# Kernel tuning notes

Hardware: AMD Instinct MI355X
Metric: run time of the kernel (lower is better)

The kernel has to match this reference:

```python
import jax, jax.numpy as jnp
import numpy as np

DIM = 1024
NUM_HEADS = 16
DIM_HEAD = 64
INNER = NUM_HEADS * DIM_HEAD  # 1024
SCALE = DIM_HEAD ** -0.5


def setup_inputs() -> dict:
    key = jax.random.key(0)
    ks = jax.random.split(key, 8)
    B, SQ, SK = 2, 2048, 4096
    x = jax.random.normal(ks[0], (B, SQ, DIM), dtype=jnp.float32)
    context = jax.random.normal(ks[1], (B, SK, DIM), dtype=jnp.float32)
    # LayerNorm params
    ln_gamma = jnp.ones((DIM,), jnp.float32)
    ln_beta = jnp.zeros((DIM,), jnp.float32)
    # Linear weights, stored as [in, out] so y = x @ W (torch Linear weight transposed)
    w_q = jax.random.normal(ks[2], (DIM, INNER), dtype=jnp.float32) / np.sqrt(DIM)
    w_kv = jax.random.normal(ks[3], (DIM, 2 * INNER), dtype=jnp.float32) / np.sqrt(DIM)
    w_out = jax.random.normal(ks[4], (INNER, DIM), dtype=jnp.float32) / np.sqrt(INNER)
    b_out = jnp.zeros((DIM,), jnp.float32)
    # torch init is 0.0 (tanh(0)=0); use a nonzero value so output/grads are nontrivial
    gate = jnp.array([0.5], jnp.float32)
    return {"x": x, "context": context, "ln_gamma": ln_gamma, "ln_beta": ln_beta,
            "w_q": w_q, "w_kv": w_kv, "w_out": w_out, "b_out": b_out, "gate": gate}


def _layernorm(x, gamma, beta, eps=1e-5):
    mu = jnp.mean(x, axis=-1, keepdims=True)
    var = jnp.mean(jnp.square(x - mu), axis=-1, keepdims=True)
    return (x - mu) * jax.lax.rsqrt(var + eps) * gamma + beta


def reference(x, context, ln_gamma, ln_beta, w_q, w_kv, w_out, b_out, gate):
    B, SQ, _ = x.shape
    SK = context.shape[1]
    xn = _layernorm(x, ln_gamma, ln_beta)
    q = (xn @ w_q).reshape(B, SQ, NUM_HEADS, DIM_HEAD)
    kv = context @ w_kv
    k, v = jnp.split(kv, 2, axis=-1)
    k = k.reshape(B, SK, NUM_HEADS, DIM_HEAD)
    v = v.reshape(B, SK, NUM_HEADS, DIM_HEAD)
    # scores: [B, H, SQ, SK]
    scores = jnp.einsum('bqhd,bkhd->bhqk', q * SCALE, k)
    attn = jax.nn.softmax(scores, axis=-1)
    out = jnp.einsum('bhqk,bkhd->bqhd', attn, v).reshape(B, SQ, INNER)
    out = out @ w_out + b_out
    return out * jnp.tanh(gate[0])
```

## Files before the change

### kernel.cpp

```cpp
#include <hip/hip_runtime.h>
#include <hip/hip_bf16.h>
#include <stdint.h>

#define DIMM  1024
#define NHEAD 16
#define DHEAD 64
#define BB    2
#define SQL   2048
#define SKL   4096
#define KVW   2048
#define NT    (SKL / 64)

typedef __attribute__((ext_vector_type(8))) short short8;
typedef __attribute__((ext_vector_type(4))) float f32x4;
typedef __attribute__((ext_vector_type(16))) float f32x16;
typedef __attribute__((ext_vector_type(4))) unsigned short us4;

typedef const __attribute__((address_space(1))) uint32_t gu32_t;
typedef __attribute__((address_space(3))) uint32_t lu32_t;

#define GLDS16(gp, lp) __builtin_amdgcn_global_load_lds((gu32_t*)(gp), (lu32_t*)(lp), 16, 0, 0)

static __device__ __forceinline__ unsigned short f2bf(float f) {
  union { float f; uint32_t u; } v; v.f = f;
  uint32_t r = v.u + 0x7fffu + ((v.u >> 16) & 1u);
  return (unsigned short)(r >> 16);
}

__global__ __launch_bounds__(256) void k_wprep(const float* __restrict__ wq,
                                               const float* __restrict__ wkv,
                                               const float* __restrict__ wot,
                                               unsigned short* __restrict__ WQT,
                                               unsigned short* __restrict__ WKVT,
                                               unsigned short* __restrict__ WOT) {
  __shared__ float tile[32][33];
  const int bid = blockIdx.x;
  const float* in; unsigned short* out; int N, bx, by;
  if (bid < 1024)      {               in = wq;  out = WQT;  N = 1024; bx = bid & 31; by = bid >> 5; }
  else if (bid < 3072) { int l = bid - 1024; in = wkv; out = WKVT; N = 2048; bx = l & 63; by = l >> 6; }
  else                 { int l = bid - 3072; in = wot; out = WOT;  N = 1024; bx = l & 31; by = l >> 5; }
  const int K = 1024;
  const int n0 = bx * 32, k0 = by * 32;
  const int tx = threadIdx.x, ty = threadIdx.y;
  #pragma unroll
  for (int i = 0; i < 4; i++)
    tile[ty + i * 8][tx] = in[(size_t)(k0 + ty + i * 8) * N + n0 + tx];
  __syncthreads();
  #pragma unroll
  for (int i = 0; i < 4; i++)
    out[(size_t)(n0 + ty + i * 8) * K + k0 + tx] = f2bf(tile[tx][ty + i * 8]);
}

__global__ __launch_bounds__(256) void k_ln(const float* __restrict__ x,
                                            const float* __restrict__ gamma,
                                            const float* __restrict__ beta,
                                            unsigned short* __restrict__ out) {
  const int row = blockIdx.x, tid = threadIdx.x;
  const float* xr = x + (size_t)row * DIMM;
  float4 v = *(const float4*)(xr + tid * 4);
  float s = v.x + v.y + v.z + v.w;
  float ss = v.x * v.x + v.y * v.y + v.z * v.z + v.w * v.w;
  #pragma unroll
  for (int m = 1; m < 64; m <<= 1) {
    s += __shfl_xor(s, m);
    ss += __shfl_xor(ss, m);
  }
  __shared__ float red[8];
  const int wid = tid >> 6, lane = tid & 63;
  if (lane == 0) { red[wid] = s; red[4 + wid] = ss; }
  __syncthreads();
  s = red[0] + red[1] + red[2] + red[3];
  ss = red[4] + red[5] + red[6] + red[7];
  float mu = s * (1.0f / DIMM);
  float var = ss * (1.0f / DIMM) - mu * mu;
  float rstd = rsqrtf(var + 1e-5f);
  float4 g = *(const float4*)(gamma + tid * 4);
  float4 bt = *(const float4*)(beta + tid * 4);
  us4 o;
  o.x = f2bf((v.x - mu) * rstd * g.x + bt.x);
  o.y = f2bf((v.y - mu) * rstd * g.y + bt.y);
  o.z = f2bf((v.z - mu) * rstd * g.z + bt.z);
  o.w = f2bf((v.w - mu) * rstd * g.w + bt.w);
  *(us4*)(out + (size_t)row * DIMM + tid * 4) = o;
}

__global__ __launch_bounds__(256) void k_proj(const float* __restrict__ ctx,
                                              const unsigned short* __restrict__ XN,
                                              const unsigned short* __restrict__ WKVT,
                                              const unsigned short* __restrict__ WQT,
                                              unsigned short* __restrict__ KVB,
                                              unsigned short* __restrict__ QB) {
  __shared__ unsigned short lA[2][128 * 32];
  __shared__ unsigned short lB[2][128 * 32];
  const int tid = threadIdx.x;
  const int wid = tid >> 6, lane = tid & 63;
  const int kg = lane >> 4, lr = lane & 15;
  const int wr = wid >> 1, wc = wid & 1;
  const int K = 1024, nt = 32;

  const int bid = blockIdx.x;
  const int xcd = bid & 7;
  const int idx = bid >> 3;
  const bool isQ = (idx >= 128);
  int im, in_, N;
  const unsigned short* Bw;
  unsigned short* Cout;
  if (isQ) { int q = idx - 128; im = xcd * 4 + (q & 3); in_ = q >> 2; Bw = WQT;  Cout = QB;  N = 1024; }
  else     {                    im = xcd * 8 + (idx & 7); in_ = idx >> 3; Bw = WKVT; Cout = KVB; N = 2048; }
  const size_t baseB = (size_t)in_ * 128 * K;
  const unsigned short* Abf = XN + (size_t)im * 128 * K;
  const float* Af = ctx + (size_t)im * 128 * K;

  int ed[2], grow[2], gcol[2];
  #pragma unroll
  for (int j = 0; j < 2; j++) {
    int e = wid * 1024 + j * 512 + lane * 8;
    ed[j] = e;
    int row = e >> 5;
    grow[j] = row;
    gcol[j] = (((e >> 3) & 3) ^ ((row >> 1) & 3)) << 3;
  }
  uint32_t awoff[4];
  #pragma unroll
  for (int p = 0; p < 4; p++) {
    int row = p * 32 + (tid >> 3);
    int g = (tid & 7) >> 1;
    awoff[p] = (uint32_t)(row * 64 + ((g ^ ((row >> 1) & 3)) << 4) + (tid & 1) * 8);
  }

  f32x4 acc[4][4];
  #pragma unroll
  for (int m = 0; m < 4; m++)
    #pragma unroll
    for (int n = 0; n < 4; n++) {
      f32x4 z = {0.0f, 0.0f, 0.0f, 0.0f};
      acc[m][n] = z;
    }

  float4 va[4];
  auto STAGE_B = [&](int bufi, int t) {
    int k0 = t << 5;
    #pragma unroll
    for (int j = 0; j < 2; j++)
      GLDS16(Bw + baseB + (size_t)grow[j] * K + k0 + gcol[j], &lB[bufi][ed[j]]);
  };
  auto STAGE_A_Q = [&](int bufi, int t) {
    int k0 = t << 5;
    #pragma unroll
    for (int j = 0; j < 2; j++)
      GLDS16(Abf + (size_t)grow[j] * K + k0 + gcol[j], &lA[bufi][ed[j]]);
  };
  auto LOAD_A_F32 = [&](int t) {
    int k0 = t << 5;
    #pragma unroll
    for (int p = 0; p < 4; p++)
      va[p] = *(const float4*)(Af + (size_t)(p * 32 + (tid >> 3)) * K + k0 + (tid & 7) * 4);
  };
  auto WRITE_A_F32 = [&](int bufi) {
    #pragma unroll
    for (int p = 0; p < 4; p++) {
      uint32_t lo, hi;
      asm("v_cvt_pk_bf16_f32 %0, %1, %2" : "=v"(lo) : "v"(va[p].x), "v"(va[p].y));
      asm("v_cvt_pk_bf16_f32 %0, %1, %2" : "=v"(hi) : "v"(va[p].z), "v"(va[p].w));
      uint2 w2; w2.x = lo; w2.y = hi;
      *(uint2*)((char*)&lA[bufi][0] + awoff[p]) = w2;
    }
  };
  auto COMPUTE = [&](int bufi) {
    short8 a[4], b[4];
    #pragma unroll
    for (int m = 0; m < 4; m++) {
      int row = wr * 64 + m * 16 + lr;
      a[m] = *(const short8*)&lA[bufi][row * 32 + ((kg ^ ((row >> 1) & 3)) << 3)];
    }
    #pragma unroll
    for (int n = 0; n < 4; n++) {
      int row = wc * 64 + n * 16 + lr;
      b[n] = *(const short8*)&lB[bufi][row * 32 + ((kg ^ ((row >> 1) & 3)) << 3)];
    }
    #pragma unroll
    for (int m = 0; m < 4; m++)
      #pragma unroll
      for (int n = 0; n < 4; n++)
        acc[m][n] = __builtin_amdgcn_mfma_f32_16x16x32_bf16(a[m], b[n], acc[m][n], 0, 0, 0);
  };

  int buf = 0;
  if (isQ) {
    STAGE_A_Q(0, 0); STAGE_B(0, 0);
    __syncthreads();
    for (int t = 0; t < nt; t++) {
      if (t + 1 < nt) { STAGE_A_Q(buf ^ 1, t + 1); STAGE_B(buf ^ 1, t + 1); }
      COMPUTE(buf);
      __syncthreads();
      buf ^= 1;
    }
  } else {
    LOAD_A_F32(0); STAGE_B(0, 0); WRITE_A_F32(0);
    __syncthreads();
    for (int t = 0; t < nt; t++) {
      if (t + 1 < nt) { LOAD_A_F32(t + 1); STAGE_B(buf ^ 1, t + 1); }
      COMPUTE(buf);
      if (t + 1 < nt) WRITE_A_F32(buf ^ 1);
      __syncthreads();
      buf ^= 1;
    }
  }

  const int r0 = im * 128 + wr * 64;
  const int c0 = in_ * 128 + wc * 64;
  #pragma unroll
  for (int m = 0; m < 4; m++)
    #pragma unroll
    for (int n = 0; n < 4; n++)
      #pragma unroll
      for (int j = 0; j < 4; j++)
        Cout[(size_t)(r0 + m * 16 + kg * 4 + j) * N + c0 + n * 16 + lr] = f2bf(acc[m][n][j]);
}

__global__ __launch_bounds__(256) void k_out(const unsigned short* __restrict__ A,
                                             const unsigned short* __restrict__ BT,
                                             float* __restrict__ C,
                                             const float* __restrict__ bias,
                                             const float* __restrict__ gate) {
  __shared__ unsigned short lA[2][64 * 32];
  __shared__ unsigned short lB[2][128 * 32];
  const int tid = threadIdx.x;
  const int wid = tid >> 6, lane = tid & 63;
  const int kg = lane >> 4, lr = lane & 15;
  const int wr = wid >> 1, wc = wid & 1;
  const int K = 1024, nt = 32, N = 1024;

  const int bid = blockIdx.x;
  const int xcd = bid & 7;
  const int idx = bid >> 3;
  const int im = xcd * 8 + (idx & 7);
  const int in_ = idx >> 3;
  const size_t baseA = (size_t)im * 64 * K;
  const size_t baseB = (size_t)in_ * 128 * K;

  int eA, arow, acol;
  {
    int e = tid * 8;
    eA = e;
    int row = e >> 5;
    arow = row; acol = (((e >> 3) & 3) ^ ((row >> 1) & 3)) << 3;
  }
  int eB[2], brow[2], bcol[2];
  #pragma unroll
  for (int j = 0; j < 2; j++) {
    int e = tid * 8 + j * 2048;
    eB[j] = e;
    int row = e >> 5;
    brow[j] = row; bcol[j] = (((e >> 3) & 3) ^ ((row >> 1) & 3)) << 3;
  }

  f32x4 acc[2][4];
  #pragma unroll
  for (int m = 0; m < 2; m++)
    #pragma unroll
    for (int n = 0; n < 4; n++) {
      f32x4 z = {0.0f, 0.0f, 0.0f, 0.0f};
      acc[m][n] = z;
    }

  auto STAGE = [&](int bufi, int t) {
    int k0 = t << 5;
    GLDS16(A + baseA + (size_t)arow * K + k0 + acol, &lA[bufi][eA]);
    #pragma unroll
    for (int j = 0; j < 2; j++)
      GLDS16(BT + baseB + (size_t)brow[j] * K + k0 + bcol[j], &lB[bufi][eB[j]]);
  };

  STAGE(0, 0);
  __syncthreads();
  int buf = 0;
  for (int t = 0; t < nt; t++) {
    if (t + 1 < nt) STAGE(buf ^ 1, t + 1);
    short8 a[2], b[4];
    #pragma unroll
    for (int m = 0; m < 2; m++) {
      int row = wr * 32 + m * 16 + lr;
      a[m] = *(const short8*)&lA[buf][row * 32 + ((kg ^ ((row >> 1) & 3)) << 3)];
    }
    #pragma unroll
    for (int n = 0; n < 4; n++) {
      int row = wc * 64 + n * 16 + lr;
      b[n] = *(const short8*)&lB[buf][row * 32 + ((kg ^ ((row >> 1) & 3)) << 3)];
    }
    #pragma unroll
    for (int m = 0; m < 2; m++)
      #pragma unroll
      for (int n = 0; n < 4; n++)
        acc[m][n] = __builtin_amdgcn_mfma_f32_16x16x32_bf16(a[m], b[n], acc[m][n], 0, 0, 0);
    __syncthreads();
    buf ^= 1;
  }

  const int r0 = im * 64 + wr * 32;
  const int c0 = in_ * 128 + wc * 64;
  float gl = tanhf(gate[0]);
  #pragma unroll
  for (int m = 0; m < 2; m++)
    #pragma unroll
    for (int n = 0; n < 4; n++)
      #pragma unroll
      for (int j = 0; j < 4; j++) {
        int col = c0 + n * 16 + lr;
        C[(size_t)(r0 + m * 16 + kg * 4 + j) * N + col] = (acc[m][n][j] + bias[col]) * gl;
      }
}

__global__ __launch_bounds__(256, 4) void k_attn(const unsigned short* __restrict__ Q,
                                                 const unsigned short* __restrict__ KV,
                                                 unsigned short* __restrict__ O) {
  __shared__ unsigned short sK[2][64 * 64];
  __shared__ unsigned short sV[2][64 * 64];

  const int tid = threadIdx.x;
  const int wave = tid >> 6, lane = tid & 63;
  const int wq = wave & 1, wk = wave >> 1;
  const int l31 = lane & 31, hi = lane >> 5;

  const int wid_b = blockIdx.x;
  const int work = (wid_b & 7) * 128 + (wid_b >> 3);
  const int qb = work & 31, bh = work >> 5;
  const int b = bh >> 4, h = bh & 15;

  const unsigned short* Qp = Q + (size_t)b * SQL * DIMM + h * DHEAD;
  const unsigned short* Kp = KV + (size_t)b * SKL * KVW + h * DHEAD;
  const unsigned short* Vp = Kp + DIMM;

  const int qr0 = qb * 64 + wq * 32;

  const unsigned short* ksrc[2]; int kdst[2];
  const unsigned short* vsrc[2]; int vdst[2];
  #pragma unroll
  for (int j = 0; j < 2; j++) {
    int e = (tid + j * 256) * 8;
    int row = e >> 6;
    int col = (((e >> 3) & 7) ^ (row & 7)) << 3;
    ksrc[j] = Kp + (size_t)row * KVW + col;
    kdst[j] = e;
    int g = tid + j * 256;
    int key = (g >> 5) * 4 + ((g >> 1) & 3);
    int d0v = ((g >> 3) & 3) * 16 + (g & 1) * 8;
    vsrc[j] = Vp + (size_t)key * KVW + d0v;
    vdst[j] = g * 8;
  }

  auto STAGE = [&](int bufi, int kt) {
    size_t off = (size_t)kt * 64 * KVW;
    #pragma unroll
    for (int j = 0; j < 2; j++) GLDS16(ksrc[j] + off, &sK[bufi][kdst[j]]);
    #pragma unroll
    for (int j = 0; j < 2; j++) GLDS16(vsrc[j] + off, &sV[bufi][vdst[j]]);
  };

  short8 qa[4];
  #pragma unroll
  for (int t = 0; t < 4; t++) {
    short8 v = *(const short8*)(Qp + (size_t)(qr0 + l31) * DIMM + t * 16 + hi * 8);
    #pragma unroll
    for (int j = 0; j < 8; j++) {
      union { float f; uint32_t u; } c;
      c.u = ((uint32_t)(unsigned short)v[j]) << 16;
      v[j] = (short)f2bf(c.f * 0.1803368801111f);
    }
    qa[t] = v;
  }

  f32x16 oacc[2];
  #pragma unroll
  for (int d2 = 0; d2 < 2; d2++)
    #pragma unroll
    for (int r = 0; r < 16; r++) oacc[d2][r] = 0.0f;
  float rs = 0.0f;

  const uint32_t sVb0 = (uint32_t)(size_t)(lu32_t*)&sV[0][0] +
                        (uint32_t)(hi * 1024 + ((lane >> 4) & 1) * 128 + (lane & 15) * 8);

  STAGE(0, 0);
  __syncthreads();

  union u4s8 { uint32_t u[4]; short8 s; };

  int buf = 0;
  for (int kt = 0; kt < NT; kt++) {
    if (kt + 1 < NT) STAGE(buf ^ 1, kt + 1);

    short8 kbf[4];
    {
      int row = wk * 32 + l31;
      #pragma unroll
      for (int t = 0; t < 4; t++) {
        int gl = t * 2 + hi;
        kbf[t] = *(const short8*)&sK[buf][row * 64 + ((gl ^ (row & 7)) << 3)];
      }
    }

    f32x16 sc;
    #pragma unroll
    for (int r = 0; r < 16; r++) sc[r] = 0.0f;
    #pragma unroll
    for (int t = 0; t < 4; t++)
      sc = __builtin_amdgcn_mfma_f32_32x32x16_bf16(kbf[t], qa[t], sc, 0, 0, 0);

    float p[16];
    #pragma unroll
    for (int r = 0; r < 16; r++) {
      p[r] = __builtin_amdgcn_exp2f(sc[r]);
      rs += p[r];
    }
    uint32_t w[8];
    #pragma unroll
    for (int i = 0; i < 8; i++)
      asm("v_cvt_pk_bf16_f32 %0, %1, %2" : "=v"(w[i]) : "v"(p[2 * i]), "v"(p[2 * i + 1]));
    asm("v_permlane32_swap_b32 %0, %1" : "+v"(w[0]), "+v"(w[2]));
    asm("v_permlane32_swap_b32 %0, %1" : "+v"(w[1]), "+v"(w[3]));
    asm("v_permlane32_swap_b32 %0, %1" : "+v"(w[4]), "+v"(w[6]));
    asm("v_permlane32_swap_b32 %0, %1" : "+v"(w[5]), "+v"(w[7]));
    u4s8 paf[2];
    paf[0].u[0] = w[0]; paf[0].u[1] = w[1]; paf[0].u[2] = w[2]; paf[0].u[3] = w[3];
    paf[1].u[0] = w[4]; paf[1].u[1] = w[5]; paf[1].u[2] = w[6]; paf[1].u[3] = w[7];

    u4s8 vb[2][2];
    {
      uint32_t tb = sVb0 + (uint32_t)(buf * 8192 + wk * 4096);
      #pragma unroll
      for (int d2 = 0; d2 < 2; d2++)
        #pragma unroll
        for (int ks = 0; ks < 2; ks++) {
          uint2 t0, t1;
          uint32_t a0 = tb + (uint32_t)(ks * 2048 + d2 * 256);
          asm volatile("ds_read_b64_tr_b16 %0, %1" : "=v"(t0) : "v"(a0));
          asm volatile("ds_read_b64_tr_b16 %0, %1" : "=v"(t1) : "v"(a0 + 512u));
          vb[d2][ks].u[0] = t0.x; vb[d2][ks].u[1] = t0.y;
          vb[d2][ks].u[2] = t1.x; vb[d2][ks].u[3] = t1.y;
        }
    }
    asm volatile("s_waitcnt lgkmcnt(0)" ::: "memory");
    __builtin_amdgcn_sched_barrier(0);

    #pragma unroll
    for (int d2 = 0; d2 < 2; d2++)
      #pragma unroll
      for (int ks = 0; ks < 2; ks++)
        oacc[d2] = __builtin_amdgcn_mfma_f32_32x32x16_bf16(paf[ks].s, vb[d2][ks].s, oacc[d2], 0, 0, 0);

    __syncthreads();
    buf ^= 1;
  }

  float* sRed = (float*)&sK[0][0];
  float* sRs  = (float*)&sV[0][0];
  if (wk == 1) {
    #pragma unroll
    for (int d2 = 0; d2 < 2; d2++)
      #pragma unroll
      for (int r = 0; r < 16; r++)
        sRed[((wq * 2 + d2) * 16 + r) * 64 + lane] = oacc[d2][r];
    sRs[wq * 64 + lane] = rs;
  }
  __syncthreads();
  if (wk == 0) {
    #pragma unroll
    for (int d2 = 0; d2 < 2; d2++)
      #pragma unroll
      for (int r = 0; r < 16; r++)
        oacc[d2][r] += sRed[((wq * 2 + d2) * 16 + r) * 64 + lane];
    float rs2 = rs + sRs[wq * 64 + lane];
    float t = rs2 + __shfl_xor(rs2, 32);
    float inv = 1.0f / t;
    float rq[16];
    #pragma unroll
    for (int r = 0; r < 16; r++) {
      int rho = (r & 3) + 8 * (r >> 2) + 4 * hi;
      rq[r] = __shfl(inv, rho);
    }
    unsigned short* Op = O + (size_t)b * SQL * DIMM + h * DHEAD;
    #pragma unroll
    for (int d2 = 0; d2 < 2; d2++)
      #pragma unroll
      for (int r = 0; r < 16; r++) {
        int rho = (r & 3) + 8 * (r >> 2) + 4 * hi;
        Op[(size_t)(qr0 + rho) * DIMM + d2 * 32 + l31] = f2bf(oacc[d2][r] * rq[r]);
      }
  }
}

extern "C" void kernel_launch(void* const* d_in, const int* in_sizes, int n_in,
                              void* d_out, int out_size, void* d_ws, size_t ws_size,
                              hipStream_t stream) {
  (void)in_sizes; (void)n_in; (void)out_size; (void)ws_size;
  const float* x     = (const float*)d_in[0];
  const float* ctx   = (const float*)d_in[1];
  const float* gamma = (const float*)d_in[2];
  const float* beta  = (const float*)d_in[3];
  const float* w_q   = (const float*)d_in[4];
  const float* w_kv  = (const float*)d_in[5];
  const float* w_out = (const float*)d_in[6];
  const float* b_out = (const float*)d_in[7];
  const float* gate  = (const float*)d_in[8];
  float* out = (float*)d_out;
  char* ws = (char*)d_ws;

  unsigned short* XN   = (unsigned short*)(ws);
  unsigned short* QB   = (unsigned short*)(ws + (8ull  << 20));
  unsigned short* KVB  = (unsigned short*)(ws + (32ull << 20));
  unsigned short* OB   = (unsigned short*)(ws + (64ull << 20));
  unsigned short* WQT  = (unsigned short*)(ws + (72ull << 20));
  unsigned short* WKVT = (unsigned short*)(ws + (74ull << 20));
  unsigned short* WOT  = (unsigned short*)(ws + (78ull << 20));

  k_wprep<<<dim3(4096), dim3(32, 8), 0, stream>>>(w_q, w_kv, w_out, WQT, WKVT, WOT);
  k_ln<<<dim3(4096), dim3(256), 0, stream>>>(x, gamma, beta, XN);
  k_proj<<<dim3(1280), dim3(256), 0, stream>>>(ctx, XN, WKVT, WQT, KVB, QB);
  k_attn<<<dim3(1024), dim3(256), 0, stream>>>(QB, KVB, OB);
  k_out<<<dim3(512), dim3(256), 0, stream>>>(OB, WOT, out, b_out, gate);
}
```

Before: 206.0 us.

## Merge prep kernels and pre-convert context to bf16 for uniform projection path

Combines weight transpose, layernorm, and a new context fp32-to-bf16 conversion into one prep launch, removing a kernel launch. The KV projection then stages its A operand with direct global-to-LDS bf16 loads instead of register fp32 loads plus in-loop conversion, so both projection paths share one pipeline. The cost is an extra write and read of a 16 MB bf16 context buffer through global memory.

```diff
diff --git a/kernel.cpp b/kernel.cpp
--- a/kernel.cpp
+++ b/kernel.cpp
@@ -27,64 +27,77 @@
   return (unsigned short)(r >> 16);
 }
 
-__global__ __launch_bounds__(256) void k_wprep(const float* __restrict__ wq,
-                                               const float* __restrict__ wkv,
-                                               const float* __restrict__ wot,
-                                               unsigned short* __restrict__ WQT,
-                                               unsigned short* __restrict__ WKVT,
-                                               unsigned short* __restrict__ WOT) {
-  __shared__ float tile[32][33];
+__global__ __launch_bounds__(256) void k_prep(const float* __restrict__ wq,
+                                              const float* __restrict__ wkv,
+                                              const float* __restrict__ wot,
+                                              const float* __restrict__ x,
+                                              const float* __restrict__ gamma,
+                                              const float* __restrict__ beta,
+                                              const float* __restrict__ ctx,
+                                              unsigned short* __restrict__ WQT,
+                                              unsigned short* __restrict__ WKVT,
+                                              unsigned short* __restrict__ WOT,
+                                              unsigned short* __restrict__ XN,
+                                              unsigned short* __restrict__ CTXB) {
   const int bid = blockIdx.x;
-  const float* in; unsigned short* out; int N, bx, by;
-  if (bid < 1024)      {               in = wq;  out = WQT;  N = 1024; bx = bid & 31; by = bid >> 5; }
-  else if (bid < 3072) { int l = bid - 1024; in = wkv; out = WKVT; N = 2048; bx = l & 63; by = l >> 6; }
-  else                 { int l = bid - 3072; in = wot; out = WOT;  N = 1024; bx = l & 31; by = l >> 5; }
-  const int K = 1024;
-  const int n0 = bx * 32, k0 = by * 32;
-  const int tx = threadIdx.x, ty = threadIdx.y;
-  #pragma unroll
-  for (int i = 0; i < 4; i++)
-    tile[ty + i * 8][tx] = in[(size_t)(k0 + ty + i * 8) * N + n0 + tx];
-  __syncthreads();
-  #pragma unroll
-  for (int i = 0; i < 4; i++)
-    out[(size_t)(n0 + ty + i * 8) * K + k0 + tx] = f2bf(tile[tx][ty + i * 8]);
-}
-
-__global__ __launch_bounds__(256) void k_ln(const float* __restrict__ x,
-                                            const float* __restrict__ gamma,
-                                            const float* __restrict__ beta,
-                                            unsigned short* __restrict__ out) {
-  const int row = blockIdx.x, tid = threadIdx.x;
-  const float* xr = x + (size_t)row * DIMM;
-  float4 v = *(const float4*)(xr + tid * 4);
-  float s = v.x + v.y + v.z + v.w;
-  float ss = v.x * v.x + v.y * v.y + v.z * v.z + v.w * v.w;
-  #pragma unroll
-  for (int m = 1; m < 64; m <<= 1) {
-    s += __shfl_xor(s, m);
-    ss += __shfl_xor(ss, m);
-  }
-  __shared__ float red[8];
-  const int wid = tid >> 6, lane = tid & 63;
-  if (lane == 0) { red[wid] = s; red[4 + wid] = ss; }
-  __syncthreads();
-  s = red[0] + red[1] + red[2] + red[3];
-  ss = red[4] + red[5] + red[6] + red[7];
-  float mu = s * (1.0f / DIMM);
-  float var = ss * (1.0f / DIMM) - mu * mu;
-  float rstd = rsqrtf(var + 1e-5f);
-  float4 g = *(const float4*)(gamma + tid * 4);
-  float4 bt = *(const float4*)(beta + tid * 4);
-  us4 o;
-  o.x = f2bf((v.x - mu) * rstd * g.x + bt.x);
-  o.y = f2bf((v.y - mu) * rstd * g.y + bt.y);
-  o.z = f2bf((v.z - mu) * rstd * g.z + bt.z);
-  o.w = f2bf((v.w - mu) * rstd * g.w + bt.w);
-  *(us4*)(out + (size_t)row * DIMM + tid * 4) = o;
-}
-
-__global__ __launch_bounds__(256) void k_proj(const float* __restrict__ ctx,
+  const int tid = threadIdx.x;
+
+  if (bid < 4096) {
+    __shared__ float tile[32][33];
+    const float* in; unsigned short* out; int N, bx, by;
+    if (bid < 1024)      {                    in = wq;  out = WQT;  N = 1024; bx = bid & 31; by = bid >> 5; }
+    else if (bid < 3072) { int l = bid - 1024; in = wkv; out = WKVT; N = 2048; bx = l & 63; by = l >> 6; }
+    else                 { int l = bid - 3072; in = wot; out = WOT;  N = 1024; bx = l & 31; by = l >> 5; }
+    const int K = 1024;
+    const int n0 = bx * 32, k0 = by * 32;
+    const int tx = tid & 31, ty = tid >> 5;
+    #pragma unroll
+    for (int i = 0; i < 4; i++)
+      tile[ty + i * 8][tx] = in[(size_t)(k0 + ty + i * 8) * N + n0 + tx];
+    __syncthreads();
+    #pragma unroll
+    for (int i = 0; i < 4; i++)
+      out[(size_t)(n0 + ty + i * 8) * K + k0 + tx] = f2bf(tile[tx][ty + i * 8]);
+  } else if (bid < 8192) {
+    const int row = bid - 4096;
+    const float* xr = x + (size_t)row * DIMM;
+    float4 v = *(const float4*)(xr + tid * 4);
+    float s = v.x + v.y + v.z + v.w;
+    float ss = v.x * v.x + v.y * v.y + v.z * v.z + v.w * v.w;
+    #pragma unroll
+    for (int m = 1; m < 64; m <<= 1) {
+      s += __shfl_xor(s, m);
+      ss += __shfl_xor(ss, m);
+    }
+    __shared__ float red[8];
+    const int wid = tid >> 6, lane = tid & 63;
+    if (lane == 0) { red[wid] = s; red[4 + wid] = ss; }
+    __syncthreads();
+    s = red[0] + red[1] + red[2] + red[3];
+    ss = red[4] + red[5] + red[6] + red[7];
+    float mu = s * (1.0f / DIMM);
+    float var = ss * (1.0f / DIMM) - mu * mu;
+    float rstd = rsqrtf(var + 1e-5f);
+    float4 g = *(const float4*)(gamma + tid * 4);
+    float4 bt = *(const float4*)(beta + tid * 4);
+    us4 o;
+    o.x = f2bf((v.x - mu) * rstd * g.x + bt.x);
+    o.y = f2bf((v.y - mu) * rstd * g.y + bt.y);
+    o.z = f2bf((v.z - mu) * rstd * g.z + bt.z);
+    o.w = f2bf((v.w - mu) * rstd * g.w + bt.w);
+    *(us4*)(XN + (size_t)row * DIMM + tid * 4) = o;
+  } else {
+    size_t i = ((size_t)(bid - 8192) * 256 + tid) * 8;
+    float4 v0 = *(const float4*)(ctx + i);
+    float4 v1 = *(const float4*)(ctx + i + 4);
+    union { us4 h[2]; short8 s; } o;
+    o.h[0].x = f2bf(v0.x); o.h[0].y = f2bf(v0.y); o.h[0].z = f2bf(v0.z); o.h[0].w = f2bf(v0.w);
+    o.h[1].x = f2bf(v1.x); o.h[1].y = f2bf(v1.y); o.h[1].z = f2bf(v1.z); o.h[1].w = f2bf(v1.w);
+    *(short8*)(CTXB + i) = o.s;
+  }
+}
+
+__global__ __launch_bounds__(256) void k_proj(const unsigned short* __restrict__ CTXB,
                                               const unsigned short* __restrict__ XN,
                                               const unsigned short* __restrict__ WKVT,
                                               const unsigned short* __restrict__ WQT,
@@ -103,13 +116,13 @@
   const int idx = bid >> 3;
   const bool isQ = (idx >= 128);
   int im, in_, N;
+  const unsigned short* Ap;
   const unsigned short* Bw;
   unsigned short* Cout;
-  if (isQ) { int q = idx - 128; im = xcd * 4 + (q & 3); in_ = q >> 2; Bw = WQT;  Cout = QB;  N = 1024; }
-  else     {                    im = xcd * 8 + (idx & 7); in_ = idx >> 3; Bw = WKVT; Cout = KVB; N = 2048; }
+  if (isQ) { int q = idx - 128; im = xcd * 4 + (q & 3);   in_ = q >> 2;   Bw = WQT;  Cout = QB;  N = 1024; Ap = XN; }
+  else     {                    im = xcd * 8 + (idx & 7); in_ = idx >> 3; Bw = WKVT; Cout = KVB; N = 2048; Ap = CTXB; }
   const size_t baseB = (size_t)in_ * 128 * K;
-  const unsigned short* Abf = XN + (size_t)im * 128 * K;
-  const float* Af = ctx + (size_t)im * 128 * K;
+  const unsigned short* Abf = Ap + (size_t)im * 128 * K;
 
   int ed[2], grow[2], gcol[2];
   #pragma unroll
@@ -120,13 +133,6 @@
     grow[j] = row;
     gcol[j] = (((e >> 3) & 3) ^ ((row >> 1) & 3)) << 3;
   }
-  uint32_t awoff[4];
-  #pragma unroll
-  for (int p = 0; p < 4; p++) {
-    int row = p * 32 + (tid >> 3);
-    int g = (tid & 7) >> 1;
-    awoff[p] = (uint32_t)(row * 64 + ((g ^ ((row >> 1) & 3)) << 4) + (tid & 1) * 8);
-  }
 
   f32x4 acc[4][4];
   #pragma unroll
@@ -137,33 +143,12 @@
       acc[m][n] = z;
     }
 
-  float4 va[4];
-  auto STAGE_B = [&](int bufi, int t) {
+  auto STAGE = [&](int bufi, int t) {
     int k0 = t << 5;
     #pragma unroll
-    for (int j = 0; j < 2; j++)
+    for (int j = 0; j < 2; j++) {
+      GLDS16(Abf + (size_t)grow[j] * K + k0 + gcol[j], &lA[bufi][ed[j]]);
       GLDS16(Bw + baseB + (size_t)grow[j] * K + k0 + gcol[j], &lB[bufi][ed[j]]);
-  };
-  auto STAGE_A_Q = [&](int bufi, int t) {
-    int k0 = t << 5;
-    #pragma unroll
-    for (int j = 0; j < 2; j++)
-      GLDS16(Abf + (size_t)grow[j] * K + k0 + gcol[j], &lA[bufi][ed[j]]);
-  };
-  auto LOAD_A_F32 = [&](int t) {
-    int k0 = t << 5;
-    #pragma unroll
-    for (int p = 0; p < 4; p++)
-      va[p] = *(const float4*)(Af + (size_t)(p * 32 + (tid >> 3)) * K + k0 + (tid & 7) * 4);
-  };
-  auto WRITE_A_F32 = [&](int bufi) {
-    #pragma unroll
-    for (int p = 0; p < 4; p++) {
-      uint32_t lo, hi;
-      asm("v_cvt_pk_bf16_f32 %0, %1, %2" : "=v"(lo) : "v"(va[p].x), "v"(va[p].y));
-      asm("v_cvt_pk_bf16_f32 %0, %1, %2" : "=v"(hi) : "v"(va[p].z), "v"(va[p].w));
-      uint2 w2; w2.x = lo; w2.y = hi;
-      *(uint2*)((char*)&lA[bufi][0] + awoff[p]) = w2;
     }
   };
   auto COMPUTE = [&](int bufi) {
@@ -185,26 +170,14 @@
         acc[m][n] = __builtin_amdgcn_mfma_f32_16x16x32_bf16(a[m], b[n], acc[m][n], 0, 0, 0);
   };
 
+  STAGE(0, 0);
+  __syncthreads();
   int buf = 0;
-  if (isQ) {
-    STAGE_A_Q(0, 0); STAGE_B(0, 0);
+  for (int t = 0; t < nt; t++) {
+    if (t + 1 < nt) STAGE(buf ^ 1, t + 1);
+    COMPUTE(buf);
     __syncthreads();
-    for (int t = 0; t < nt; t++) {
-      if (t + 1 < nt) { STAGE_A_Q(buf ^ 1, t + 1); STAGE_B(buf ^ 1, t + 1); }
-      COMPUTE(buf);
-      __syncthreads();
-      buf ^= 1;
-    }
-  } else {
-    LOAD_A_F32(0); STAGE_B(0, 0); WRITE_A_F32(0);
-    __syncthreads();
-    for (int t = 0; t < nt; t++) {
-      if (t + 1 < nt) { LOAD_A_F32(t + 1); STAGE_B(buf ^ 1, t + 1); }
-      COMPUTE(buf);
-      if (t + 1 < nt) WRITE_A_F32(buf ^ 1);
-      __syncthreads();
-      buf ^= 1;
-    }
+    buf ^= 1;
   }
 
   const int r0 = im * 128 + wr * 64;
@@ -507,15 +480,16 @@
 
   unsigned short* XN   = (unsigned short*)(ws);
   unsigned short* QB   = (unsigned short*)(ws + (8ull  << 20));
+  unsigned short* CTXB = (unsigned short*)(ws + (16ull << 20));
   unsigned short* KVB  = (unsigned short*)(ws + (32ull << 20));
   unsigned short* OB   = (unsigned short*)(ws + (64ull << 20));
   unsigned short* WQT  = (unsigned short*)(ws + (72ull << 20));
   unsigned short* WKVT = (unsigned short*)(ws + (74ull << 20));
   unsigned short* WOT  = (unsigned short*)(ws + (78ull << 20));
 
-  k_wprep<<<dim3(4096), dim3(32, 8), 0, stream>>>(w_q, w_kv, w_out, WQT, WKVT, WOT);
-  k_ln<<<dim3(4096), dim3(256), 0, stream>>>(x, gamma, beta, XN);
-  k_proj<<<dim3(1280), dim3(256), 0, stream>>>(ctx, XN, WKVT, WQT, KVB, QB);
+  k_prep<<<dim3(12288), dim3(256), 0, stream>>>(w_q, w_kv, w_out, x, gamma, beta, ctx,
+                                                WQT, WKVT, WOT, XN, CTXB);
+  k_proj<<<dim3(1280), dim3(256), 0, stream>>>(CTXB, XN, WKVT, WQT, KVB, QB);
   k_attn<<<dim3(1024), dim3(256), 0, stream>>>(QB, KVB, OB);
   k_out<<<dim3(512), dim3(256), 0, stream>>>(OB, WOT, out, b_out, gate);
 }
```

Measured after the change: 200.9 us (median of 3 runs). 2.5% less time.
